# Kernel tuning notes

Measured on AMD Instinct MI355X. Metric: run time of the kernel, lower is better.

Reference implementation:

```python
import jax, jax.numpy as jnp
import numpy as np

D_MODEL = 1024
NUM_HEADS = 16
HEAD_DIM = D_MODEL // NUM_HEADS


def setup_inputs() -> dict:
    key = jax.random.key(0)
    ks = jax.random.split(key, 11)
    B, S = 4, 2048
    s = 1.0 / np.sqrt(D_MODEL)
    inp = {
        "query": jax.random.normal(ks[0], (B, S, D_MODEL), jnp.float32),
        "key": jax.random.normal(ks[1], (B, S, D_MODEL), jnp.float32),
        "value": jax.random.normal(ks[2], (B, S, D_MODEL), jnp.float32),
        "Wq": jax.random.normal(ks[3], (D_MODEL, D_MODEL), jnp.float32) * s,
        "bq": jnp.zeros((D_MODEL,), jnp.float32),
        "Wk": jax.random.normal(ks[4], (D_MODEL, D_MODEL), jnp.float32) * s,
        "bk": jnp.zeros((D_MODEL,), jnp.float32),
        "Wv": jax.random.normal(ks[5], (D_MODEL, D_MODEL), jnp.float32) * s,
        "bv": jnp.zeros((D_MODEL,), jnp.float32),
        "Wo": jax.random.normal(ks[6], (D_MODEL, D_MODEL), jnp.float32) * s,
        "bo": jnp.zeros((D_MODEL,), jnp.float32),
    }
    return inp


def reference(query, key, value, Wq, bq, Wk, bk, Wv, bv, Wo, bo):
    B, S, _ = query.shape
    def proj(x, W, b):  # [B,S,D] -> [B,H,S,hd]
        y = jnp.einsum("bsd,ed->bse", x, W) + b
        return y.reshape(B, -1, NUM_HEADS, HEAD_DIM).transpose(0, 2, 1, 3)
    q = proj(query, Wq, bq)
    k = proj(key, Wk, bk)
    v = proj(value, Wv, bv)
    scores = jnp.einsum("bhqd,bhkd->bhqk", q, k) / np.sqrt(HEAD_DIM).astype(jnp.float32)
    attn = jax.nn.softmax(scores, axis=-1)
    out = jnp.einsum("bhqk,bhkd->bhqd", attn, v)
    out = out.transpose(0, 2, 1, 3).reshape(B, -1, D_MODEL)
    return jnp.einsum("bsd,ed->bse", out, Wo) + bo
```

## Files before the change

kernel.cpp:

```cpp
#include <hip/hip_runtime.h>
#include <math.h>

#define DM    1024
#define NH    16
#define HD    64
#define SEQ   2048
#define BATCH 4
#define TOKENS (BATCH * SEQ)

typedef _Float16 half2v __attribute__((ext_vector_type(2)));
typedef __fp16   fp16x2 __attribute__((ext_vector_type(2)));
typedef _Float16 half4  __attribute__((ext_vector_type(4)));
typedef _Float16 half8  __attribute__((ext_vector_type(8)));
typedef float    f32x4  __attribute__((ext_vector_type(4)));
typedef float    f32x16 __attribute__((ext_vector_type(16)));
typedef unsigned int u32x2 __attribute__((ext_vector_type(2)));
typedef unsigned int u32x4 __attribute__((ext_vector_type(4)));

typedef const __attribute__((address_space(1))) void* gas_p;
typedef __attribute__((address_space(3))) void*       las_p;

__device__ __forceinline__ void gload_lds16(const void* g, void* l) {
    __builtin_amdgcn_global_load_lds((gas_p)g, (las_p)l, 16, 0, 0);
}

__device__ __forceinline__ unsigned pack2u(float a, float b) {
    fp16x2 r = __builtin_amdgcn_cvt_pkrtz(a, b);
    return __builtin_bit_cast(unsigned, r);
}

#define MFMA16(a, b, c) __builtin_amdgcn_mfma_f32_16x16x32_f16((a), (b), (c), 0, 0, 0)
#define MFMA32(a, b, c) __builtin_amdgcn_mfma_f32_32x32x16_f16((a), (b), (c), 0, 0, 0)

__global__ __launch_bounds__(256) void cvt_all(
    const float* __restrict__ q, const float* __restrict__ k,
    const float* __restrict__ v, const float* __restrict__ wq,
    const float* __restrict__ wk, const float* __restrict__ wv,
    const float* __restrict__ wo, _Float16* __restrict__ dst)
{
    const size_t TD = (size_t)TOKENS * DM, WD = (size_t)DM * DM;
    const size_t i = ((size_t)blockIdx.x * 256 + threadIdx.x) * 4;
    const float* s; size_t off;
    if      (i <     TD)          { s = q;  off = i; }
    else if (i < 2 * TD)          { s = k;  off = i - TD; }
    else if (i < 3 * TD)          { s = v;  off = i - 2 * TD; }
    else if (i < 3 * TD + WD)     { s = wq; off = i - 3 * TD; }
    else if (i < 3 * TD + 2 * WD) { s = wk; off = i - 3 * TD - WD; }
    else if (i < 3 * TD + 3 * WD) { s = wv; off = i - 3 * TD - 2 * WD; }
    else                          { s = wo; off = i - 3 * TD - 3 * WD; }
    const float4 x = *(const float4*)(s + off);
    half4 h = { (_Float16)x.x, (_Float16)x.y, (_Float16)x.z, (_Float16)x.w };
    *(half4*)(dst + i) = h;
}

__global__ __launch_bounds__(256) void qkv_gemm(
    const _Float16* __restrict__ Abase, const _Float16* __restrict__ Wbase,
    const float* __restrict__ bq, const float* __restrict__ bk,
    const float* __restrict__ bv, _Float16* __restrict__ Cbase, float qscale)
{
    __shared__ __align__(16) _Float16 As[128 * 32];
    __shared__ __align__(16) _Float16 Ws[128 * 32];

    const int z = blockIdx.z;
    const size_t TD = (size_t)TOKENS * DM, WD = (size_t)DM * DM;
    const _Float16* A = Abase + (size_t)z * TD;
    const _Float16* W = Wbase + (size_t)z * WD;
    const float* bias = (z == 0) ? bq : (z == 1) ? bk : bv;
    _Float16* C = Cbase + (size_t)z * TD;
    const float scale = (z == 0) ? qscale : 1.0f;

    const int t = threadIdx.x;
    const int w = t >> 6, l = t & 63;
    const int tx = l & 15, quad = l >> 4;
    const int m0 = blockIdx.x * 128, n0 = blockIdx.y * 128;
    const int wm = (w & 1) * 64, wn = (w >> 1) * 64;
    const int srow = t >> 2, schk = t & 3;

    const _Float16* Ag = A + (size_t)m0 * DM;
    const _Float16* Wg = W + (size_t)n0 * DM;

    f32x4 acc[4][4] = {};

    for (int k0 = 0; k0 < DM; k0 += 32) {
        __syncthreads();
        #pragma unroll
        for (int i = 0; i < 2; ++i) {
            gload_lds16(Ag + (size_t)(i * 64 + srow) * DM + k0 + schk * 8,
                        As + (size_t)(i * 256 + (t & ~63)) * 8);
            gload_lds16(Wg + (size_t)(i * 64 + srow) * DM + k0 + schk * 8,
                        Ws + (size_t)(i * 256 + (t & ~63)) * 8);
        }
        __syncthreads();

        half8 af[4], bf[4];
        #pragma unroll
        for (int mt = 0; mt < 4; ++mt)
            af[mt] = *(const half8*)(As + (wm + mt * 16 + tx) * 32 + quad * 8);
        #pragma unroll
        for (int nt = 0; nt < 4; ++nt)
            bf[nt] = *(const half8*)(Ws + (wn + nt * 16 + tx) * 32 + quad * 8);
        #pragma unroll
        for (int mt = 0; mt < 4; ++mt)
            #pragma unroll
            for (int nt = 0; nt < 4; ++nt)
                acc[mt][nt] = MFMA16(af[mt], bf[nt], acc[mt][nt]);
    }

    float bsv[4];
    #pragma unroll
    for (int nt = 0; nt < 4; ++nt) bsv[nt] = bias[n0 + wn + nt * 16 + tx];

    #pragma unroll
    for (int mt = 0; mt < 4; ++mt) {
        #pragma unroll
        for (int nt = 0; nt < 4; ++nt) {
            const int n = n0 + wn + nt * 16 + tx;
            const int mr0 = m0 + wm + mt * 16 + quad * 4;
            const int h = n >> 6, d = n & 63;
            if (z < 2) {
                #pragma unroll
                for (int r = 0; r < 4; ++r) {
                    const int m = mr0 + r;
                    const int b = m >> 11, s = m & (SEQ - 1);
                    const float vv = (acc[mt][nt][r] + bsv[nt]) * scale;
                    C[(((size_t)b * NH + h) * SEQ + s) * HD + d] = (_Float16)vv;
                }
            } else {
                const int b = mr0 >> 11, s0 = mr0 & (SEQ - 1);
                half4 hv = { (_Float16)(acc[mt][nt][0] + bsv[nt]),
                             (_Float16)(acc[mt][nt][1] + bsv[nt]),
                             (_Float16)(acc[mt][nt][2] + bsv[nt]),
                             (_Float16)(acc[mt][nt][3] + bsv[nt]) };
                *(half4*)(C + (((size_t)b * NH + h) * HD + d) * SEQ + s0) = hv;
            }
        }
    }
}

__global__ __launch_bounds__(256) void out_gemm(
    const _Float16* __restrict__ A, const _Float16* __restrict__ W,
    const float* __restrict__ bias, float* __restrict__ C)
{
    __shared__ __align__(16) _Float16 As[128 * 32];
    __shared__ __align__(16) _Float16 Ws[128 * 32];

    const int t = threadIdx.x;
    const int w = t >> 6, l = t & 63;
    const int tx = l & 15, quad = l >> 4;
    const int m0 = blockIdx.x * 128, n0 = blockIdx.y * 128;
    const int wm = (w & 1) * 64, wn = (w >> 1) * 64;
    const int srow = t >> 2, schk = t & 3;

    const _Float16* Ag = A + (size_t)m0 * DM;
    const _Float16* Wg = W + (size_t)n0 * DM;

    f32x4 acc[4][4] = {};

    for (int k0 = 0; k0 < DM; k0 += 32) {
        __syncthreads();
        #pragma unroll
        for (int i = 0; i < 2; ++i) {
            gload_lds16(Ag + (size_t)(i * 64 + srow) * DM + k0 + schk * 8,
                        As + (size_t)(i * 256 + (t & ~63)) * 8);
            gload_lds16(Wg + (size_t)(i * 64 + srow) * DM + k0 + schk * 8,
                        Ws + (size_t)(i * 256 + (t & ~63)) * 8);
        }
        __syncthreads();

        half8 af[4], bf[4];
        #pragma unroll
        for (int mt = 0; mt < 4; ++mt)
            af[mt] = *(const half8*)(As + (wm + mt * 16 + tx) * 32 + quad * 8);
        #pragma unroll
        for (int nt = 0; nt < 4; ++nt)
            bf[nt] = *(const half8*)(Ws + (wn + nt * 16 + tx) * 32 + quad * 8);
        #pragma unroll
        for (int mt = 0; mt < 4; ++mt)
            #pragma unroll
            for (int nt = 0; nt < 4; ++nt)
                acc[mt][nt] = MFMA16(af[mt], bf[nt], acc[mt][nt]);
    }

    float bsv[4];
    #pragma unroll
    for (int nt = 0; nt < 4; ++nt) bsv[nt] = bias[n0 + wn + nt * 16 + tx];

    #pragma unroll
    for (int mt = 0; mt < 4; ++mt)
        #pragma unroll
        for (int nt = 0; nt < 4; ++nt) {
            const int n = n0 + wn + nt * 16 + tx;
            const int mr0 = m0 + wm + mt * 16 + quad * 4;
            #pragma unroll
            for (int r = 0; r < 4; ++r)
                C[(size_t)(mr0 + r) * DM + n] = acc[mt][nt][r] + bsv[nt];
        }
}

__global__ __launch_bounds__(128, 2) void flash16(
    const _Float16* __restrict__ Q, const _Float16* __restrict__ K,
    const _Float16* __restrict__ Vt, _Float16* __restrict__ AO)
{
    __shared__ __align__(16) char pool[34816];
    __shared__ float lW[128];

    const int t = threadIdx.x, w = t >> 6, l = t & 63;
    const int lid = l & 31, hl = l >> 5;

    const int bid = blockIdx.x;
    const int xcd = bid & 7, loc = bid >> 3;
    const int bh = xcd * 8 + (loc >> 4);
    const int q0 = (loc & 15) * 128;
    const int b = bh >> 4, h = bh & 15;

    const _Float16* Qg = Q + ((size_t)bh * SEQ + q0 + w * 64) * HD;
    const _Float16* Kg = K + (size_t)bh * SEQ * HD;
    const _Float16* Vg = Vt + (size_t)bh * HD * SEQ;

    const int srow = l >> 3;
    const int schk = (l & 7) ^ srow;

    half8 Qf[2][4];
    #pragma unroll
    for (int qq = 0; qq < 2; ++qq)
        #pragma unroll
        for (int ks = 0; ks < 4; ++ks)
            Qf[qq][ks] = *(const half8*)(Qg + (size_t)(qq * 32 + lid) * HD + ks * 16 + hl * 8);

    f32x16 Oa[2][2] = {};
    float l2[2] = {0.f, 0.f};
    const half2v one2 = { (_Float16)1.0f, (_Float16)1.0f };

    {
        _Float16* KL = (_Float16*)(pool);
        _Float16* VL = (_Float16*)(pool + 16384);
        #pragma unroll
        for (int jj = 0; jj < 4; ++jj) {
            const int j = w + jj * 2;
            const int row = 8 * j + srow;
            gload_lds16(Kg + (size_t)row * HD + schk * 8, KL + j * 512);
            gload_lds16(Vg + (size_t)row * SEQ + schk * 8, VL + j * 512);
        }
    }

    for (int it = 0; it < SEQ / 64; ++it) {
        __syncthreads();

        if (it < SEQ / 64 - 1) {
            const int kb = (it + 1) * 64;
            _Float16* KL = (_Float16*)(pool + ((it + 1) & 1) * 8192);
            _Float16* VL = (_Float16*)(pool + 16384 + ((it + 1) & 1) * 8192);
            #pragma unroll
            for (int jj = 0; jj < 4; ++jj) {
                const int j = w + jj * 2;
                const int row = 8 * j + srow;
                gload_lds16(Kg + (size_t)(kb + row) * HD + schk * 8, KL + j * 512);
                gload_lds16(Vg + (size_t)row * SEQ + kb + schk * 8, VL + j * 512);
            }
        }

        const _Float16* KL = (const _Float16*)(pool + (it & 1) * 8192);
        const _Float16* VL = (const _Float16*)(pool + 16384 + (it & 1) * 8192);

        half8 kf[2][4];
        #pragma unroll
        for (int kt = 0; kt < 2; ++kt)
            #pragma unroll
            for (int ks = 0; ks < 4; ++ks)
                kf[kt][ks] = *(const half8*)(KL + (kt * 32 + lid) * 64 +
                                             (((ks * 2 + hl) ^ (lid & 7)) * 8));

        half8 pa[2][4];
        #pragma unroll
        for (int qq = 0; qq < 2; ++qq) {
            f32x16 sacc[2];
            __builtin_amdgcn_s_setprio(1);
            #pragma unroll
            for (int kt = 0; kt < 2; ++kt) {
                f32x16 s = {};
                #pragma unroll
                for (int ks = 0; ks < 4; ++ks)
                    s = MFMA32(kf[kt][ks], Qf[qq][ks], s);
                sacc[kt] = s;
            }
            __builtin_amdgcn_s_setprio(0);

            unsigned cf[2][4][2];
            #pragma unroll
            for (int kt = 0; kt < 2; ++kt)
                #pragma unroll
                for (int g = 0; g < 4; ++g) {
                    const float p0 = __builtin_amdgcn_exp2f(sacc[kt][g * 4 + 0]);
                    const float p1 = __builtin_amdgcn_exp2f(sacc[kt][g * 4 + 1]);
                    const float p2 = __builtin_amdgcn_exp2f(sacc[kt][g * 4 + 2]);
                    const float p3 = __builtin_amdgcn_exp2f(sacc[kt][g * 4 + 3]);
                    const unsigned ca = pack2u(p0, p1);
                    const unsigned cb = pack2u(p2, p3);
                    l2[qq] = __builtin_amdgcn_fdot2(__builtin_bit_cast(half2v, ca), one2, l2[qq], false);
                    l2[qq] = __builtin_amdgcn_fdot2(__builtin_bit_cast(half2v, cb), one2, l2[qq], false);
                    cf[kt][g][0] = ca;
                    cf[kt][g][1] = cb;
                }

            #pragma unroll
            for (int kstep = 0; kstep < 4; ++kstep) {
                const int kt = kstep >> 1, g0 = (kstep & 1) * 2;
                const u32x2 r0 = __builtin_amdgcn_permlane32_swap(
                    cf[kt][g0][0], cf[kt][g0 + 1][0], false, false);
                const u32x2 r1 = __builtin_amdgcn_permlane32_swap(
                    cf[kt][g0][1], cf[kt][g0 + 1][1], false, false);
                const u32x4 pw = { r0[0], r1[0], r0[1], r1[1] };
                pa[qq][kstep] = __builtin_bit_cast(half8, pw);
            }
        }

        half8 vf[4][2];
        #pragma unroll
        for (int kstep = 0; kstep < 4; ++kstep)
            #pragma unroll
            for (int dt = 0; dt < 2; ++dt)
                vf[kstep][dt] = *(const half8*)(VL + (dt * 32 + lid) * 64 +
                                                (((kstep * 2 + hl) ^ (lid & 7)) * 8));

        __builtin_amdgcn_s_setprio(1);
        #pragma unroll
        for (int kstep = 0; kstep < 4; ++kstep)
            #pragma unroll
            for (int qq = 0; qq < 2; ++qq)
                #pragma unroll
                for (int dt = 0; dt < 2; ++dt)
                    Oa[qq][dt] = MFMA32(pa[qq][kstep], vf[kstep][dt], Oa[qq][dt]);
        __builtin_amdgcn_s_setprio(0);
    }

    #pragma unroll
    for (int qq = 0; qq < 2; ++qq)
        l2[qq] += __shfl_xor(l2[qq], 32, 64);
    if (l < 32) {
        lW[w * 64 + l] = l2[0];
        lW[w * 64 + 32 + l] = l2[1];
    }
    __syncthreads();

    float* Ob = (float*)pool;
    #pragma unroll
    for (int qq = 0; qq < 2; ++qq)
        #pragma unroll
        for (int dt = 0; dt < 2; ++dt)
            #pragma unroll
            for (int g = 0; g < 4; ++g)
                #pragma unroll
                for (int r = 0; r < 4; ++r)
                    Ob[(w * 64 + qq * 32 + g * 8 + hl * 4 + r) * 68 + dt * 32 + lid] =
                        Oa[qq][dt][g * 4 + r];
    __syncthreads();

    {
        const int row = t;
        const float inv = 1.0f / lW[row];
        _Float16* dst = AO + ((size_t)b * SEQ + q0 + row) * DM + h * HD;
        #pragma unroll
        for (int j = 0; j < 64; j += 8) {
            const f32x4 o0 = *(const f32x4*)(Ob + row * 68 + j);
            const f32x4 o1 = *(const f32x4*)(Ob + row * 68 + j + 4);
            half8 hv = { (_Float16)(o0[0] * inv), (_Float16)(o0[1] * inv),
                         (_Float16)(o0[2] * inv), (_Float16)(o0[3] * inv),
                         (_Float16)(o1[0] * inv), (_Float16)(o1[1] * inv),
                         (_Float16)(o1[2] * inv), (_Float16)(o1[3] * inv) };
            *(half8*)(dst + j) = hv;
        }
    }
}

extern "C" void kernel_launch(void* const* d_in, const int* in_sizes, int n_in,
                              void* d_out, int out_size, void* d_ws, size_t ws_size,
                              hipStream_t stream)
{
    const float* q  = (const float*)d_in[0];
    const float* k  = (const float*)d_in[1];
    const float* v  = (const float*)d_in[2];
    const float* Wq = (const float*)d_in[3];
    const float* bq = (const float*)d_in[4];
    const float* Wk = (const float*)d_in[5];
    const float* bk = (const float*)d_in[6];
    const float* Wv = (const float*)d_in[7];
    const float* bv = (const float*)d_in[8];
    const float* Wo = (const float*)d_in[9];
    const float* bo = (const float*)d_in[10];
    float* out = (float*)d_out;

    const size_t TD = (size_t)TOKENS * DM;
    const size_t WD = (size_t)DM * DM;
    _Float16* ws = (_Float16*)d_ws;
    _Float16* cvtbase = ws;
    _Float16* q16  = ws;
    _Float16* wq16 = ws + 3 * TD;
    _Float16* wo16 = wq16 + 3 * WD;
    _Float16* Qw   = ws + 3 * TD + 4 * WD;
    _Float16* Kw   = Qw + TD;
    _Float16* Vtw  = Kw + TD;
    _Float16* AOw  = Vtw + TD;

    const int gC = (int)((3 * TD + 4 * WD) / 4 / 256);
    cvt_all<<<gC, 256, 0, stream>>>(q, k, v, Wq, Wk, Wv, Wo, cvtbase);

    const float qscale = 0.18033688011112042f;
    qkv_gemm<<<dim3(TOKENS / 128, DM / 128, 3), 256, 0, stream>>>(
        q16, wq16, bq, bk, bv, Qw, qscale);

    flash16<<<dim3((SEQ / 128) * BATCH * NH), 128, 0, stream>>>(Qw, Kw, Vtw, AOw);

    out_gemm<<<dim3(TOKENS / 128, DM / 128, 1), 256, 0, stream>>>(AOw, wo16, bo, out);
}
```

Before: 344.6 us.

## Split KV sequence across wave pairs in flash kernel and merge partial outputs

The flash attention block grows from 2 to 4 waves. Each pair of waves processes half of the key/value sequence for the same 128 query rows, using its own double-buffered LDS staging area. The partial O accumulators and row sums are merged through LDS in two phases before normalisation and the fp16 store. This halves the serial KV loop length per block and raises the wave count, at the cost of 64KB LDS per block, which may cap resident blocks per CU, plus an extra LDS merge step.

```diff
diff --git a/kernel.cpp b/kernel.cpp
--- a/kernel.cpp
+++ b/kernel.cpp
@@ -197,15 +197,16 @@
         }
 }
 
-__global__ __launch_bounds__(128, 2) void flash16(
+__global__ __launch_bounds__(256, 4) void flash16(
     const _Float16* __restrict__ Q, const _Float16* __restrict__ K,
     const _Float16* __restrict__ Vt, _Float16* __restrict__ AO)
 {
-    __shared__ __align__(16) char pool[34816];
+    __shared__ __align__(16) char pool[65536];
     __shared__ float lW[128];
 
     const int t = threadIdx.x, w = t >> 6, l = t & 63;
     const int lid = l & 31, hl = l >> 5;
+    const int p = w >> 1, wp = w & 1;
 
     const int bid = blockIdx.x;
     const int xcd = bid & 7, loc = bid >> 3;
@@ -213,12 +214,15 @@
     const int q0 = (loc & 15) * 128;
     const int b = bh >> 4, h = bh & 15;
 
-    const _Float16* Qg = Q + ((size_t)bh * SEQ + q0 + w * 64) * HD;
-    const _Float16* Kg = K + (size_t)bh * SEQ * HD;
-    const _Float16* Vg = Vt + (size_t)bh * HD * SEQ;
+    const _Float16* Qg = Q + ((size_t)bh * SEQ + q0 + wp * 64) * HD;
+    const _Float16* Kg = K + ((size_t)bh * SEQ + p * 1024) * HD;
+    const _Float16* Vg = Vt + (size_t)bh * HD * SEQ + p * 1024;
 
     const int srow = l >> 3;
     const int schk = (l & 7) ^ srow;
+
+    char* const Kst = pool + p * 16384;
+    char* const Vst = pool + 32768 + p * 16384;
 
     half8 Qf[2][4];
     #pragma unroll
@@ -232,35 +236,36 @@
     const half2v one2 = { (_Float16)1.0f, (_Float16)1.0f };
 
     {
-        _Float16* KL = (_Float16*)(pool);
-        _Float16* VL = (_Float16*)(pool + 16384);
+        _Float16* KL = (_Float16*)Kst;
+        _Float16* VL = (_Float16*)Vst;
         #pragma unroll
         for (int jj = 0; jj < 4; ++jj) {
-            const int j = w + jj * 2;
+            const int j = wp + jj * 2;
             const int row = 8 * j + srow;
             gload_lds16(Kg + (size_t)row * HD + schk * 8, KL + j * 512);
             gload_lds16(Vg + (size_t)row * SEQ + schk * 8, VL + j * 512);
         }
     }
 
-    for (int it = 0; it < SEQ / 64; ++it) {
+    const int NIT = SEQ / 2 / 64;
+    for (int it = 0; it < NIT; ++it) {
         __syncthreads();
 
-        if (it < SEQ / 64 - 1) {
+        if (it < NIT - 1) {
             const int kb = (it + 1) * 64;
-            _Float16* KL = (_Float16*)(pool + ((it + 1) & 1) * 8192);
-            _Float16* VL = (_Float16*)(pool + 16384 + ((it + 1) & 1) * 8192);
+            _Float16* KL = (_Float16*)(Kst + ((it + 1) & 1) * 8192);
+            _Float16* VL = (_Float16*)(Vst + ((it + 1) & 1) * 8192);
             #pragma unroll
             for (int jj = 0; jj < 4; ++jj) {
-                const int j = w + jj * 2;
+                const int j = wp + jj * 2;
                 const int row = 8 * j + srow;
                 gload_lds16(Kg + (size_t)(kb + row) * HD + schk * 8, KL + j * 512);
                 gload_lds16(Vg + (size_t)row * SEQ + kb + schk * 8, VL + j * 512);
             }
         }
 
-        const _Float16* KL = (const _Float16*)(pool + (it & 1) * 8192);
-        const _Float16* VL = (const _Float16*)(pool + 16384 + (it & 1) * 8192);
+        const _Float16* KL = (const _Float16*)(Kst + (it & 1) * 8192);
+        const _Float16* VL = (const _Float16*)(Vst + (it & 1) * 8192);
 
         half8 kf[2][4];
         #pragma unroll
@@ -336,33 +341,53 @@
     #pragma unroll
     for (int qq = 0; qq < 2; ++qq)
         l2[qq] += __shfl_xor(l2[qq], 32, 64);
-    if (l < 32) {
-        lW[w * 64 + l] = l2[0];
-        lW[w * 64 + 32 + l] = l2[1];
-    }
+
     __syncthreads();
 
     float* Ob = (float*)pool;
-    #pragma unroll
-    for (int qq = 0; qq < 2; ++qq)
-        #pragma unroll
-        for (int dt = 0; dt < 2; ++dt)
-            #pragma unroll
-            for (int g = 0; g < 4; ++g)
-                #pragma unroll
-                for (int r = 0; r < 4; ++r)
-                    Ob[(w * 64 + qq * 32 + g * 8 + hl * 4 + r) * 68 + dt * 32 + lid] =
-                        Oa[qq][dt][g * 4 + r];
+    if (p == 0) {
+        #pragma unroll
+        for (int qq = 0; qq < 2; ++qq)
+            #pragma unroll
+            for (int dt = 0; dt < 2; ++dt)
+                #pragma unroll
+                for (int g = 0; g < 4; ++g)
+                    #pragma unroll
+                    for (int r = 0; r < 4; ++r)
+                        Ob[(wp * 64 + qq * 32 + g * 8 + hl * 4 + r) * 68 + dt * 32 + lid] =
+                            Oa[qq][dt][g * 4 + r];
+        if (l < 32) {
+            lW[wp * 64 + l] = l2[0];
+            lW[wp * 64 + 32 + l] = l2[1];
+        }
+    }
     __syncthreads();
+    if (p == 1) {
+        #pragma unroll
+        for (int qq = 0; qq < 2; ++qq)
+            #pragma unroll
+            for (int dt = 0; dt < 2; ++dt)
+                #pragma unroll
+                for (int g = 0; g < 4; ++g)
+                    #pragma unroll
+                    for (int r = 0; r < 4; ++r)
+                        Ob[(wp * 64 + qq * 32 + g * 8 + hl * 4 + r) * 68 + dt * 32 + lid] +=
+                            Oa[qq][dt][g * 4 + r];
+        if (l < 32) {
+            lW[wp * 64 + l] += l2[0];
+            lW[wp * 64 + 32 + l] += l2[1];
+        }
+    }
+    __syncthreads();
 
     {
-        const int row = t;
+        const int row = t >> 1, cb = (t & 1) * 32;
         const float inv = 1.0f / lW[row];
-        _Float16* dst = AO + ((size_t)b * SEQ + q0 + row) * DM + h * HD;
-        #pragma unroll
-        for (int j = 0; j < 64; j += 8) {
-            const f32x4 o0 = *(const f32x4*)(Ob + row * 68 + j);
-            const f32x4 o1 = *(const f32x4*)(Ob + row * 68 + j + 4);
+        _Float16* dst = AO + ((size_t)b * SEQ + q0 + row) * DM + h * HD + cb;
+        #pragma unroll
+        for (int j = 0; j < 32; j += 8) {
+            const f32x4 o0 = *(const f32x4*)(Ob + row * 68 + cb + j);
+            const f32x4 o1 = *(const f32x4*)(Ob + row * 68 + cb + j + 4);
             half8 hv = { (_Float16)(o0[0] * inv), (_Float16)(o0[1] * inv),
                          (_Float16)(o0[2] * inv), (_Float16)(o0[3] * inv),
                          (_Float16)(o1[0] * inv), (_Float16)(o1[1] * inv),
@@ -408,7 +433,7 @@
     qkv_gemm<<<dim3(TOKENS / 128, DM / 128, 3), 256, 0, stream>>>(
         q16, wq16, bq, bk, bv, Qw, qscale);
 
-    flash16<<<dim3((SEQ / 128) * BATCH * NH), 128, 0, stream>>>(Qw, Kw, Vtw, AOw);
+    flash16<<<dim3((SEQ / 128) * BATCH * NH), 256, 0, stream>>>(Qw, Kw, Vtw, AOw);
 
     out_gemm<<<dim3(TOKENS / 128, DM / 128, 1), 256, 0, stream>>>(AOw, wo16, bo, out);
 }
```

Result: slower. 383.0 us (+11.1%).

## Drop LDS staging in flash attention and load K/V directly per wave

Applied to the files above, without the earlier changes.

The flash attention kernel goes from 128-thread blocks to single-wave 64-thread blocks. Each wave now reads K and transposed V tiles straight from global memory into registers, replacing the double-buffered global_load_lds pipeline and its per-iteration barriers. The aim is to remove LDS traffic and synchronisation and to raise the number of resident blocks. In exchange, K/V are no longer shared between waves and no longer prefetched, so global/L2 traffic doubles and load latency sits on the critical path. The output staging uses a 69-float row stride, which makes the 16-byte vector LDS reads misaligned.

```diff
diff --git a/kernel.cpp b/kernel.cpp
--- a/kernel.cpp
+++ b/kernel.cpp
@@ -197,28 +197,25 @@
         }
 }
 
-__global__ __launch_bounds__(128, 2) void flash16(
+__global__ __launch_bounds__(64, 2) void flash16(
     const _Float16* __restrict__ Q, const _Float16* __restrict__ K,
     const _Float16* __restrict__ Vt, _Float16* __restrict__ AO)
 {
-    __shared__ __align__(16) char pool[34816];
-    __shared__ float lW[128];
-
-    const int t = threadIdx.x, w = t >> 6, l = t & 63;
+    __shared__ __align__(16) float Ob[64 * 69];
+    __shared__ float lw[64];
+
+    const int l = threadIdx.x;
     const int lid = l & 31, hl = l >> 5;
 
     const int bid = blockIdx.x;
     const int xcd = bid & 7, loc = bid >> 3;
-    const int bh = xcd * 8 + (loc >> 4);
-    const int q0 = (loc & 15) * 128;
+    const int bh = xcd * 8 + (loc >> 5);
+    const int q0 = (loc & 31) * 64;
     const int b = bh >> 4, h = bh & 15;
 
-    const _Float16* Qg = Q + ((size_t)bh * SEQ + q0 + w * 64) * HD;
+    const _Float16* Qg = Q + ((size_t)bh * SEQ + q0) * HD;
     const _Float16* Kg = K + (size_t)bh * SEQ * HD;
     const _Float16* Vg = Vt + (size_t)bh * HD * SEQ;
-
-    const int srow = l >> 3;
-    const int schk = (l & 7) ^ srow;
 
     half8 Qf[2][4];
     #pragma unroll
@@ -231,44 +228,24 @@
     float l2[2] = {0.f, 0.f};
     const half2v one2 = { (_Float16)1.0f, (_Float16)1.0f };
 
-    {
-        _Float16* KL = (_Float16*)(pool);
-        _Float16* VL = (_Float16*)(pool + 16384);
-        #pragma unroll
-        for (int jj = 0; jj < 4; ++jj) {
-            const int j = w + jj * 2;
-            const int row = 8 * j + srow;
-            gload_lds16(Kg + (size_t)row * HD + schk * 8, KL + j * 512);
-            gload_lds16(Vg + (size_t)row * SEQ + schk * 8, VL + j * 512);
-        }
-    }
-
     for (int it = 0; it < SEQ / 64; ++it) {
-        __syncthreads();
-
-        if (it < SEQ / 64 - 1) {
-            const int kb = (it + 1) * 64;
-            _Float16* KL = (_Float16*)(pool + ((it + 1) & 1) * 8192);
-            _Float16* VL = (_Float16*)(pool + 16384 + ((it + 1) & 1) * 8192);
-            #pragma unroll
-            for (int jj = 0; jj < 4; ++jj) {
-                const int j = w + jj * 2;
-                const int row = 8 * j + srow;
-                gload_lds16(Kg + (size_t)(kb + row) * HD + schk * 8, KL + j * 512);
-                gload_lds16(Vg + (size_t)row * SEQ + kb + schk * 8, VL + j * 512);
-            }
-        }
-
-        const _Float16* KL = (const _Float16*)(pool + (it & 1) * 8192);
-        const _Float16* VL = (const _Float16*)(pool + 16384 + (it & 1) * 8192);
+        const int kb = it * 64;
 
         half8 kf[2][4];
         #pragma unroll
         for (int kt = 0; kt < 2; ++kt)
             #pragma unroll
             for (int ks = 0; ks < 4; ++ks)
-                kf[kt][ks] = *(const half8*)(KL + (kt * 32 + lid) * 64 +
-                                             (((ks * 2 + hl) ^ (lid & 7)) * 8));
+                kf[kt][ks] = *(const half8*)(Kg + (size_t)(kb + kt * 32 + lid) * HD +
+                                             ks * 16 + hl * 8);
+
+        half8 vf[4][2];
+        #pragma unroll
+        for (int kstep = 0; kstep < 4; ++kstep)
+            #pragma unroll
+            for (int dt = 0; dt < 2; ++dt)
+                vf[kstep][dt] = *(const half8*)(Vg + (size_t)(dt * 32 + lid) * SEQ +
+                                                kb + kstep * 16 + hl * 8);
 
         half8 pa[2][4];
         #pragma unroll
@@ -314,14 +291,6 @@
             }
         }
 
-        half8 vf[4][2];
-        #pragma unroll
-        for (int kstep = 0; kstep < 4; ++kstep)
-            #pragma unroll
-            for (int dt = 0; dt < 2; ++dt)
-                vf[kstep][dt] = *(const half8*)(VL + (dt * 32 + lid) * 64 +
-                                                (((kstep * 2 + hl) ^ (lid & 7)) * 8));
-
         __builtin_amdgcn_s_setprio(1);
         #pragma unroll
         for (int kstep = 0; kstep < 4; ++kstep)
@@ -337,12 +306,10 @@
     for (int qq = 0; qq < 2; ++qq)
         l2[qq] += __shfl_xor(l2[qq], 32, 64);
     if (l < 32) {
-        lW[w * 64 + l] = l2[0];
-        lW[w * 64 + 32 + l] = l2[1];
-    }
-    __syncthreads();
-
-    float* Ob = (float*)pool;
+        lw[l] = l2[0];
+        lw[32 + l] = l2[1];
+    }
+
     #pragma unroll
     for (int qq = 0; qq < 2; ++qq)
         #pragma unroll
@@ -351,18 +318,17 @@
             for (int g = 0; g < 4; ++g)
                 #pragma unroll
                 for (int r = 0; r < 4; ++r)
-                    Ob[(w * 64 + qq * 32 + g * 8 + hl * 4 + r) * 68 + dt * 32 + lid] =
+                    Ob[(qq * 32 + g * 8 + hl * 4 + r) * 69 + dt * 32 + lid] =
                         Oa[qq][dt][g * 4 + r];
     __syncthreads();
 
     {
-        const int row = t;
-        const float inv = 1.0f / lW[row];
-        _Float16* dst = AO + ((size_t)b * SEQ + q0 + row) * DM + h * HD;
+        const float inv = 1.0f / lw[l];
+        _Float16* dst = AO + ((size_t)b * SEQ + q0 + l) * DM + h * HD;
         #pragma unroll
         for (int j = 0; j < 64; j += 8) {
-            const f32x4 o0 = *(const f32x4*)(Ob + row * 68 + j);
-            const f32x4 o1 = *(const f32x4*)(Ob + row * 68 + j + 4);
+            const f32x4 o0 = *(const f32x4*)(Ob + l * 69 + j);
+            const f32x4 o1 = *(const f32x4*)(Ob + l * 69 + j + 4);
             half8 hv = { (_Float16)(o0[0] * inv), (_Float16)(o0[1] * inv),
                          (_Float16)(o0[2] * inv), (_Float16)(o0[3] * inv),
                          (_Float16)(o1[0] * inv), (_Float16)(o1[1] * inv),
@@ -408,7 +374,7 @@
     qkv_gemm<<<dim3(TOKENS / 128, DM / 128, 3), 256, 0, stream>>>(
         q16, wq16, bq, bk, bv, Qw, qscale);
 
-    flash16<<<dim3((SEQ / 128) * BATCH * NH), 128, 0, stream>>>(Qw, Kw, Vtw, AOw);
+    flash16<<<dim3((SEQ / 64) * BATCH * NH), 64, 0, stream>>>(Qw, Kw, Vtw, AOw);
 
     out_gemm<<<dim3(TOKENS / 128, DM / 128, 1), 256, 0, stream>>>(AOw, wo16, bo, out);
 }
```

After: 381.6 us. 10.7% more time.
